# Optimization experiments

Measured on AMD Instinct MI355X. Metric: run time of the kernel, lower is better.

Reference implementation:

```python
import jax, jax.numpy as jnp
import numpy as np
from jax import lax

TOP_K = 4
N_GROUP = 4
TOPK_GROUP = 2
ROUTED_SCALE = 2.5
NEG_INF = -1e9


def setup_inputs() -> dict:
    key = jax.random.key(0)
    ks = jax.random.split(key, 6)
    B, S, H, I, E = 2, 2048, 1024, 512, 16
    x = jax.random.normal(ks[0], (B, S, H), dtype=jnp.float32)
    router_weight = jax.random.normal(ks[1], (E, H), dtype=jnp.float32) * 0.02
    router_bias = jnp.zeros((E,), dtype=jnp.float32)
    w_gate = jax.random.normal(ks[2], (E, I, H), dtype=jnp.float32) * 0.02
    w_up = jax.random.normal(ks[3], (E, I, H), dtype=jnp.float32) * 0.02
    w_down = jax.random.normal(ks[4], (E, H, I), dtype=jnp.float32) * 0.02
    return {"x": x, "router_weight": router_weight, "router_bias": router_bias,
            "w_gate": w_gate, "w_up": w_up, "w_down": w_down}


def _route(xf, router_weight, router_bias):
    # DeepSeek-V3 sigmoid router with group-limited top-k.
    T = xf.shape[0]
    E = router_weight.shape[0]
    logits = xf @ router_weight.T                      # [T, E]
    scores = jax.nn.sigmoid(logits)                    # [T, E]
    s_choice = scores + router_bias                    # bias used only for selection
    per_group = E // N_GROUP
    sg = s_choice.reshape(T, N_GROUP, per_group)
    group_scores = lax.top_k(sg, 2)[0].sum(-1)         # [T, n_group] sum of top-2
    _, gidx = lax.top_k(group_scores, TOPK_GROUP)      # [T, topk_group]
    gmask = jnp.zeros((T, N_GROUP), dtype=bool).at[jnp.arange(T)[:, None], gidx].set(True)
    masked = jnp.where(gmask[:, :, None], sg, NEG_INF).reshape(T, E)
    _, topk_idx = lax.top_k(masked, TOP_K)             # [T, top_k]
    w = jnp.take_along_axis(scores, topk_idx, axis=1)  # original sigmoid scores
    w = w / (w.sum(-1, keepdims=True) + 1e-20) * ROUTED_SCALE
    combine = jnp.zeros((T, E), dtype=xf.dtype).at[jnp.arange(T)[:, None], topk_idx].add(w)
    return combine


def reference(x, router_weight, router_bias, w_gate, w_up, w_down):
    B, S, H = x.shape
    E = w_gate.shape[0]
    xf = x.reshape(-1, H)                              # [T, H]
    combine = _route(xf, router_weight, router_bias)   # [T, E]
    # Grouped-GEMM SwiGLU experts expressed as per-expert dense GEMMs with
    # combine-weighted accumulation (same math as sort+grouped-mm+scatter).
    out = jnp.zeros_like(xf)
    for e in range(E):
        g = xf @ w_gate[e].T                           # [T, I]
        u = xf @ w_up[e].T                             # [T, I]
        y_e = (jax.nn.silu(g) * u) @ w_down[e].T       # [T, H]
        out = out + combine[:, e:e + 1] * y_e
    return out.reshape(B, S, H)
```

## Files before the change

kernel.cpp:

```cpp
#include <hip/hip_runtime.h>
#include <stdint.h>

#define T_TOK   4096
#define H_DIM   1024
#define I_DIM   512
#define E_EXP   16
#define TOPK    4
#define NTILEMAX 144

typedef __attribute__((ext_vector_type(8))) short bf16x8;
typedef __attribute__((ext_vector_type(4))) float f32x4;
typedef __attribute__((ext_vector_type(8))) unsigned short ushort8;

__device__ __forceinline__ unsigned short f2bf(float f) {
  unsigned u = __float_as_uint(f);
  u = u + 0x7fffu + ((u >> 16) & 1u);
  return (unsigned short)(u >> 16);
}
__device__ __forceinline__ float bf2f(unsigned short s) {
  return __uint_as_float(((unsigned)s) << 16);
}

__device__ __forceinline__ unsigned cvtpk(float lo, float hi) {
  unsigned r;
  asm("v_cvt_pk_bf16_f32 %0, %1, %2" : "=v"(r) : "v"(lo), "v"(hi));
  return r;
}

__device__ __forceinline__ void gload_lds16(const void* g, void* l) {
  __builtin_amdgcn_global_load_lds(
      (const __attribute__((address_space(1))) unsigned int*)g,
      (__attribute__((address_space(3))) unsigned int*)l, 16, 0, 0);
}

__global__ __launch_bounds__(256) void cvt_wd_kernel(
    const float* __restrict__ wd, unsigned short* __restrict__ wdb) {
  const int tid0 = blockIdx.x * blockDim.x + threadIdx.x;
  const int stride = gridDim.x * blockDim.x;
  const int n8 = E_EXP * H_DIM * I_DIM / 8;
  for (int i = tid0; i < n8; i += stride) {
    float4 v0 = ((const float4*)wd)[2 * i];
    float4 v1 = ((const float4*)wd)[2 * i + 1];
    ushort8 o;
    o[0] = f2bf(v0.x); o[1] = f2bf(v0.y); o[2] = f2bf(v0.z); o[3] = f2bf(v0.w);
    o[4] = f2bf(v1.x); o[5] = f2bf(v1.y); o[6] = f2bf(v1.z); o[7] = f2bf(v1.w);
    ((ushort8*)wdb)[i] = o;
  }
}

__global__ __launch_bounds__(256) void logits_sel_kernel(
    const float* __restrict__ x, const float* __restrict__ rw,
    const float* __restrict__ rb, unsigned short* __restrict__ xb,
    int* __restrict__ tidx, float* __restrict__ tw) {
  const int t = blockIdx.x * 4 + (threadIdx.x >> 6);
  const int lane = threadIdx.x & 63;
  const float* xr = x + (size_t)t * H_DIM;

  float4 xv[4];
#pragma unroll
  for (int i = 0; i < 4; ++i) xv[i] = ((const float4*)xr)[i * 64 + lane];

  unsigned short* xrow = xb + (size_t)t * H_DIM;
#pragma unroll
  for (int i = 0; i < 4; ++i) {
    ushort4 o;
    o.x = f2bf(xv[i].x); o.y = f2bf(xv[i].y);
    o.z = f2bf(xv[i].z); o.w = f2bf(xv[i].w);
    ((ushort4*)xrow)[i * 64 + lane] = o;
  }

  float myl[E_EXP];
#pragma unroll
  for (int g = 0; g < 4; ++g) {
    float acc[4] = {0.f, 0.f, 0.f, 0.f};
#pragma unroll
    for (int e4 = 0; e4 < 4; ++e4) {
      const float* wrow = rw + (size_t)(g * 4 + e4) * H_DIM;
#pragma unroll
      for (int i = 0; i < 4; ++i) {
        float4 wv = ((const float4*)wrow)[i * 64 + lane];
        acc[e4] = fmaf(xv[i].x, wv.x, acc[e4]);
        acc[e4] = fmaf(xv[i].y, wv.y, acc[e4]);
        acc[e4] = fmaf(xv[i].z, wv.z, acc[e4]);
        acc[e4] = fmaf(xv[i].w, wv.w, acc[e4]);
      }
    }
#pragma unroll
    for (int e4 = 0; e4 < 4; ++e4) {
#pragma unroll
      for (int off = 32; off > 0; off >>= 1) acc[e4] += __shfl_down(acc[e4], off, 64);
      myl[g * 4 + e4] = acc[e4];
    }
  }
  if (lane != 0) return;

  float sc[E_EXP], sch[E_EXP];
#pragma unroll
  for (int e = 0; e < E_EXP; ++e) {
    sc[e] = 1.f / (1.f + expf(-myl[e]));
    sch[e] = sc[e] + rb[e];
  }

  float gsum[4];
#pragma unroll
  for (int g = 0; g < 4; ++g) {
    float m1 = -3e38f, m2 = -3e38f;
#pragma unroll
    for (int j = 0; j < 4; ++j) {
      float v = sch[g * 4 + j];
      if (v > m1) { m2 = m1; m1 = v; } else if (v > m2) { m2 = v; }
    }
    gsum[g] = m1 + m2;
  }
  int g1 = 0;
  for (int g = 1; g < 4; ++g) if (gsum[g] > gsum[g1]) g1 = g;
  int g2 = -1;
  for (int g = 0; g < 4; ++g)
    if (g != g1 && (g2 < 0 || gsum[g] > gsum[g2])) g2 = g;

  float cand[E_EXP];
#pragma unroll
  for (int e = 0; e < E_EXP; ++e)
    cand[e] = ((e >> 2) == g1 || (e >> 2) == g2) ? sch[e] : -1e9f;

  int idx[TOPK]; float wv[TOPK]; float wsum = 0.f;
#pragma unroll
  for (int k = 0; k < TOPK; ++k) {
    int bi = 0; float bv = cand[0];
#pragma unroll
    for (int e = 1; e < E_EXP; ++e) if (cand[e] > bv) { bv = cand[e]; bi = e; }
    idx[k] = bi; cand[bi] = -3e38f;
    wv[k] = sc[bi];
    wsum += wv[k];
  }
  float scale = 2.5f / (wsum + 1e-20f);
#pragma unroll
  for (int k = 0; k < TOPK; ++k) {
    tidx[t * 4 + k] = idx[k];
    tw[t * 4 + k] = wv[k] * scale;
  }
}

__global__ __launch_bounds__(256) void plan_kernel(
    const int* __restrict__ tidx, int* __restrict__ offg,
    int* __restrict__ toffg, int* __restrict__ rowmap,
    int* __restrict__ rowtok) {
  const int e = blockIdx.x, tid = threadIdx.x;
  const int lane = tid & 63, wv = tid >> 6;
  __shared__ int histo[E_EXP];
  __shared__ int wsum[4];
  __shared__ int srun;
  if (tid < E_EXP) histo[tid] = 0;
  if (tid == 0) srun = 0;
  __syncthreads();
  for (int i = tid; i < T_TOK * TOPK; i += 256)
    atomicAdd(&histo[tidx[i]], 1);
  __syncthreads();

  if (e == 0 && tid == 0) {
    int a = 0, tt = 0;
    for (int q = 0; q < E_EXP; ++q) {
      offg[q] = a; toffg[q] = tt;
      a += histo[q];
      tt += (histo[q] + 127) >> 7;
    }
    offg[E_EXP] = a; toffg[E_EXP] = tt;
  }
  int base = 0;
  for (int q = 0; q < e; ++q) base += histo[q];

  for (int c = 0; c < T_TOK * TOPK / 256; ++c) {
    const int i = c * 256 + tid;
    const bool f = (tidx[i] == e);
    unsigned long long m = __ballot(f);
    int wpre = __popcll(m & ((1ull << lane) - 1ull));
    if (lane == 63) wsum[wv] = wpre + (f ? 1 : 0);
    __syncthreads();
    const int run = srun;
    int pre = 0, tot = 0;
#pragma unroll
    for (int w = 0; w < 4; ++w) {
      int v = wsum[w];
      if (w < wv) pre += v;
      tot += v;
    }
    if (f) {
      const int pos = base + run + pre + wpre;
      rowmap[i] = pos;
      rowtok[pos] = i >> 2;
    }
    __syncthreads();
    if (tid == 0) srun = run + tot;
  }
}

__device__ __forceinline__ int find_expert(const int* __restrict__ toff, int tile) {
  int e = 0;
#pragma unroll
  for (int q = 1; q <= E_EXP; ++q) e += (toff[q] <= tile);
  return e;
}

__global__ __launch_bounds__(256, 3) void gateup_kernel(
    const unsigned short* __restrict__ xbf,
    const float* __restrict__ wgf,
    const float* __restrict__ wuf,
    const int* __restrict__ rowtok, const int* __restrict__ off,
    const int* __restrict__ toff,
    unsigned short* __restrict__ hbuf) {
  const int bid = (int)blockIdx.x;
  const int work = (bid & 7) * NTILEMAX + (bid >> 3);
  const int tile = work >> 3, tn = work & 7;
  if (tile >= toff[E_EXP]) return;
  const int e = find_expert(toff, tile);
  const int tm = tile - toff[e];
  const int seg0 = off[e];
  const int nrows = off[e + 1] - seg0;

  __shared__ __align__(16) unsigned short As[128 * 64];
  __shared__ __align__(16) unsigned short Gs[64 * 64];
  __shared__ __align__(16) unsigned short Us[64 * 64];
  __shared__ int ids[128];

  const int tid = threadIdx.x;
  if (tid < 128) {
    int r = tm * 128 + tid;
    ids[tid] = rowtok[seg0 + (r < nrows ? r : 0)];
  }
  __syncthreads();

  const int col8 = tid & 7;
  const int r0 = tid >> 3;
  const int csrc = (col8 ^ (r0 & 7)) * 8;
  const int bcol = col8 * 8;
  const int bdst = (col8 ^ (r0 & 7)) * 8;
  int tokA[4];
#pragma unroll
  for (int j = 0; j < 4; ++j) tokA[j] = ids[j * 32 + r0];

  const float* wg = wgf + (size_t)e * I_DIM * H_DIM + (size_t)(tn * 64) * H_DIM;
  const float* wu = wuf + (size_t)e * I_DIM * H_DIM + (size_t)(tn * 64) * H_DIM;

  f32x4 accg[4][2], accu[4][2];
#pragma unroll
  for (int m = 0; m < 4; ++m)
#pragma unroll
    for (int n = 0; n < 2; ++n) { accg[m][n] = (f32x4)0.f; accu[m][n] = (f32x4)0.f; }

  const int lane = tid & 63, wid = tid >> 6;
  const int wr = wid >> 1, wc = wid & 1;
  const int frow = lane & 15, fr7 = frow & 7;
  const int kc = lane >> 4;

  const int NT = H_DIM / 64;
  float4 Bg[2][2], Bu[2][2];

  auto loadB = [&](int kt) {
#pragma unroll
    for (int j = 0; j < 2; ++j) {
      const float* gs = wg + (size_t)(j * 32 + r0) * H_DIM + kt * 64 + bcol;
      const float* us = wu + (size_t)(j * 32 + r0) * H_DIM + kt * 64 + bcol;
      Bg[j][0] = ((const float4*)gs)[0]; Bg[j][1] = ((const float4*)gs)[1];
      Bu[j][0] = ((const float4*)us)[0]; Bu[j][1] = ((const float4*)us)[1];
    }
  };

  loadB(0);
  for (int kt = 0; kt < NT; ++kt) {
    const int kbA = kt * 64 + csrc;
#pragma unroll
    for (int j = 0; j < 4; ++j)
      gload_lds16(xbf + ((size_t)tokA[j] * H_DIM + kbA), (char*)As + (j * 256 + tid) * 16);
#pragma unroll
    for (int j = 0; j < 2; ++j) {
      const int row = j * 32 + r0;
      uint4 gw, uw;
      gw.x = cvtpk(Bg[j][0].x, Bg[j][0].y); gw.y = cvtpk(Bg[j][0].z, Bg[j][0].w);
      gw.z = cvtpk(Bg[j][1].x, Bg[j][1].y); gw.w = cvtpk(Bg[j][1].z, Bg[j][1].w);
      uw.x = cvtpk(Bu[j][0].x, Bu[j][0].y); uw.y = cvtpk(Bu[j][0].z, Bu[j][0].w);
      uw.z = cvtpk(Bu[j][1].x, Bu[j][1].y); uw.w = cvtpk(Bu[j][1].z, Bu[j][1].w);
      *(uint4*)&Gs[row * 64 + bdst] = gw;
      *(uint4*)&Us[row * 64 + bdst] = uw;
    }
    __syncthreads();
    if (kt + 1 < NT) loadB(kt + 1);
    __builtin_amdgcn_sched_barrier(0);
#pragma unroll
    for (int kk = 0; kk < 2; ++kk) {
      const int swz = ((kk * 4 + kc) ^ fr7) * 8;
      bf16x8 af[4], bg[2], bu[2];
#pragma unroll
      for (int m = 0; m < 4; ++m)
        af[m] = *(const bf16x8*)&As[(wr * 64 + m * 16 + frow) * 64 + swz];
#pragma unroll
      for (int n = 0; n < 2; ++n) {
        bg[n] = *(const bf16x8*)&Gs[(wc * 32 + n * 16 + frow) * 64 + swz];
        bu[n] = *(const bf16x8*)&Us[(wc * 32 + n * 16 + frow) * 64 + swz];
      }
#pragma unroll
      for (int m = 0; m < 4; ++m)
#pragma unroll
        for (int n = 0; n < 2; ++n) {
          accg[m][n] = __builtin_amdgcn_mfma_f32_16x16x32_bf16(af[m], bg[n], accg[m][n], 0, 0, 0);
          accu[m][n] = __builtin_amdgcn_mfma_f32_16x16x32_bf16(af[m], bu[n], accu[m][n], 0, 0, 0);
        }
    }
    __builtin_amdgcn_sched_barrier(0);
    __builtin_amdgcn_s_barrier();
    __builtin_amdgcn_sched_barrier(0);
  }

  const int lr = (lane >> 4) * 4, lc = lane & 15;
#pragma unroll
  for (int m = 0; m < 4; ++m) {
#pragma unroll
    for (int j = 0; j < 4; ++j) {
      int r = tm * 128 + wr * 64 + m * 16 + lr + j;
      if (r < nrows) {
        size_t rowoff = (size_t)(seg0 + r) * I_DIM;
#pragma unroll
        for (int n = 0; n < 2; ++n) {
          float g = accg[m][n][j];
          float u = accu[m][n][j];
          float hv = g / (1.f + __expf(-g)) * u;
          hbuf[rowoff + tn * 64 + wc * 32 + n * 16 + lc] = f2bf(hv);
        }
      }
    }
  }
}

__global__ __launch_bounds__(256, 3) void down_kernel(
    const unsigned short* __restrict__ hbuf,
    const unsigned short* __restrict__ wdbf,
    const int* __restrict__ off, const int* __restrict__ toff,
    unsigned short* __restrict__ ybuf) {
  const int bid = (int)blockIdx.x;
  const int work = (bid & 7) * NTILEMAX + (bid >> 3);
  const int tile = work >> 3, tn = work & 7;
  if (tile >= toff[E_EXP]) return;
  const int e = find_expert(toff, tile);
  const int tm = tile - toff[e];
  const int seg0 = off[e];
  const int nrows = off[e + 1] - seg0;

  __shared__ __align__(16) unsigned short As[128 * 64];
  __shared__ __align__(16) unsigned short Bs[128 * 64];

  const int tid = threadIdx.x;
  const int col8 = tid & 7;
  const int r0 = tid >> 3;
  const int csrc = (col8 ^ (r0 & 7)) * 8;
  int rowA[4];
#pragma unroll
  for (int j = 0; j < 4; ++j) {
    int r = tm * 128 + j * 32 + r0;
    rowA[j] = seg0 + (r < nrows ? r : nrows - 1);
  }
  const unsigned short* wd = wdbf + (size_t)e * H_DIM * I_DIM + (size_t)(tn * 128) * I_DIM;

  f32x4 acc[4][4];
#pragma unroll
  for (int m = 0; m < 4; ++m)
#pragma unroll
    for (int n = 0; n < 4; ++n) acc[m][n] = (f32x4)0.f;

  const int lane = tid & 63, wid = tid >> 6;
  const int wr = wid >> 1, wc = wid & 1;
  const int frow = lane & 15, fr7 = frow & 7;
  const int kc = lane >> 4;

  for (int kt = 0; kt < I_DIM / 64; ++kt) {
    const int kb = kt * 64 + csrc;
    __syncthreads();
#pragma unroll
    for (int j = 0; j < 4; ++j) {
      gload_lds16(hbuf + ((size_t)rowA[j] * I_DIM + kb), (char*)As + (j * 256 + tid) * 16);
      gload_lds16(wd + ((size_t)(j * 32 + r0) * I_DIM + kb), (char*)Bs + (j * 256 + tid) * 16);
    }
    __syncthreads();
#pragma unroll
    for (int kk = 0; kk < 2; ++kk) {
      const int swz = ((kk * 4 + kc) ^ fr7) * 8;
      bf16x8 af[4], bw[4];
#pragma unroll
      for (int m = 0; m < 4; ++m)
        af[m] = *(const bf16x8*)&As[(wr * 64 + m * 16 + frow) * 64 + swz];
#pragma unroll
      for (int n = 0; n < 4; ++n)
        bw[n] = *(const bf16x8*)&Bs[(wc * 64 + n * 16 + frow) * 64 + swz];
#pragma unroll
      for (int m = 0; m < 4; ++m)
#pragma unroll
        for (int n = 0; n < 4; ++n)
          acc[m][n] = __builtin_amdgcn_mfma_f32_16x16x32_bf16(af[m], bw[n], acc[m][n], 0, 0, 0);
    }
  }

  const int lr = (lane >> 4) * 4, lc = lane & 15;
#pragma unroll
  for (int m = 0; m < 4; ++m) {
#pragma unroll
    for (int j = 0; j < 4; ++j) {
      int r = tm * 128 + wr * 64 + m * 16 + lr + j;
      if (r < nrows) {
        size_t rowoff = (size_t)(seg0 + r) * H_DIM;
#pragma unroll
        for (int n = 0; n < 4; ++n)
          ybuf[rowoff + tn * 128 + wc * 64 + n * 16 + lc] = f2bf(acc[m][n][j]);
      }
    }
  }
}

__global__ __launch_bounds__(256) void combine_kernel(
    const unsigned short* __restrict__ ybuf, const int* __restrict__ rowmap,
    const float* __restrict__ tw, float* __restrict__ out) {
  int t = blockIdx.x, tid = threadIdx.x;
  __shared__ int rloc[4];
  __shared__ float wloc[4];
  if (tid < 4) { rloc[tid] = rowmap[t * 4 + tid]; wloc[tid] = tw[t * 4 + tid]; }
  __syncthreads();
  int c = tid * 4;
  float4 a = {0.f, 0.f, 0.f, 0.f};
#pragma unroll
  for (int k = 0; k < 4; ++k) {
    ushort4 v = *(const ushort4*)&ybuf[(size_t)rloc[k] * H_DIM + c];
    float w = wloc[k];
    a.x += w * bf2f(v.x); a.y += w * bf2f(v.y);
    a.z += w * bf2f(v.z); a.w += w * bf2f(v.w);
  }
  *(float4*)&out[(size_t)t * H_DIM + c] = a;
}

extern "C" void kernel_launch(void* const* d_in, const int* in_sizes, int n_in,
                              void* d_out, int out_size, void* d_ws, size_t ws_size,
                              hipStream_t stream) {
  (void)in_sizes; (void)n_in; (void)out_size; (void)ws_size;
  const float* x  = (const float*)d_in[0];
  const float* rw = (const float*)d_in[1];
  const float* rb = (const float*)d_in[2];
  const float* wg = (const float*)d_in[3];
  const float* wu = (const float*)d_in[4];
  const float* wd = (const float*)d_in[5];
  float* out = (float*)d_out;

  char* base = (char*)d_ws;
  size_t o = 0;
  auto alloc = [&](size_t b) -> void* {
    void* p = base + o;
    o += (b + 255) & ~(size_t)255;
    return p;
  };
  unsigned short* xbf   = (unsigned short*)alloc((size_t)T_TOK * H_DIM * 2);
  unsigned short* wdbf  = (unsigned short*)alloc((size_t)E_EXP * H_DIM * I_DIM * 2);
  unsigned short* hbuf  = (unsigned short*)alloc((size_t)T_TOK * TOPK * I_DIM * 2);
  unsigned short* ybuf  = (unsigned short*)alloc((size_t)T_TOK * TOPK * H_DIM * 2);
  int*   tidx   = (int*)alloc((size_t)T_TOK * TOPK * 4);
  float* tw     = (float*)alloc((size_t)T_TOK * TOPK * 4);
  int*   rowmap = (int*)alloc((size_t)T_TOK * TOPK * 4);
  int*   rowtok = (int*)alloc((size_t)T_TOK * TOPK * 4);
  int*   offb   = (int*)alloc(256);
  int*   toffb  = (int*)alloc(256);

  cvt_wd_kernel<<<2048, 256, 0, stream>>>(wd, wdbf);
  logits_sel_kernel<<<T_TOK / 4, 256, 0, stream>>>(x, rw, rb, xbf, tidx, tw);
  plan_kernel<<<E_EXP, 256, 0, stream>>>(tidx, offb, toffb, rowmap, rowtok);

  gateup_kernel<<<8 * NTILEMAX, 256, 0, stream>>>(xbf, wg, wu, rowtok, offb, toffb, hbuf);
  down_kernel<<<8 * NTILEMAX, 256, 0, stream>>>(hbuf, wdbf, offb, toffb, ybuf);
  combine_kernel<<<T_TOK, 256, 0, stream>>>(ybuf, rowmap, tw, out);
}
```

Measured before the change: 159.2 us.

## Double M-tile to 256 rows and convert down weights in-kernel

Raises the per-block row tile from 128 to 256 in both expert GEMMs, so each block reuses every weight tile across twice as many tokens, and gives each wave a full 64-row strip with more accumulators. The separate fp32-to-bf16 conversion pass over the down-projection weights is removed. The down kernel now loads fp32 weights into registers one step ahead and converts them into shared memory, as the gate/up kernel already does. This costs more registers and LDS (occupancy hint drops to 2), leaves fewer blocks, and wastes more padding rows on small experts.

```diff
diff --git a/kernel.cpp b/kernel.cpp
--- a/kernel.cpp
+++ b/kernel.cpp
@@ -6,11 +6,10 @@
 #define I_DIM   512
 #define E_EXP   16
 #define TOPK    4
-#define NTILEMAX 144
+#define TILEMAX 80
 
 typedef __attribute__((ext_vector_type(8))) short bf16x8;
 typedef __attribute__((ext_vector_type(4))) float f32x4;
-typedef __attribute__((ext_vector_type(8))) unsigned short ushort8;
 
 __device__ __forceinline__ unsigned short f2bf(float f) {
   unsigned u = __float_as_uint(f);
@@ -31,21 +30,6 @@
   __builtin_amdgcn_global_load_lds(
       (const __attribute__((address_space(1))) unsigned int*)g,
       (__attribute__((address_space(3))) unsigned int*)l, 16, 0, 0);
-}
-
-__global__ __launch_bounds__(256) void cvt_wd_kernel(
-    const float* __restrict__ wd, unsigned short* __restrict__ wdb) {
-  const int tid0 = blockIdx.x * blockDim.x + threadIdx.x;
-  const int stride = gridDim.x * blockDim.x;
-  const int n8 = E_EXP * H_DIM * I_DIM / 8;
-  for (int i = tid0; i < n8; i += stride) {
-    float4 v0 = ((const float4*)wd)[2 * i];
-    float4 v1 = ((const float4*)wd)[2 * i + 1];
-    ushort8 o;
-    o[0] = f2bf(v0.x); o[1] = f2bf(v0.y); o[2] = f2bf(v0.z); o[3] = f2bf(v0.w);
-    o[4] = f2bf(v1.x); o[5] = f2bf(v1.y); o[6] = f2bf(v1.z); o[7] = f2bf(v1.w);
-    ((ushort8*)wdb)[i] = o;
-  }
 }
 
 __global__ __launch_bounds__(256) void logits_sel_kernel(
@@ -162,7 +146,7 @@
     for (int q = 0; q < E_EXP; ++q) {
       offg[q] = a; toffg[q] = tt;
       a += histo[q];
-      tt += (histo[q] + 127) >> 7;
+      tt += (histo[q] + 255) >> 8;
     }
     offg[E_EXP] = a; toffg[E_EXP] = tt;
   }
@@ -201,7 +185,7 @@
   return e;
 }
 
-__global__ __launch_bounds__(256, 3) void gateup_kernel(
+__global__ __launch_bounds__(256, 2) void gateup_kernel(
     const unsigned short* __restrict__ xbf,
     const float* __restrict__ wgf,
     const float* __restrict__ wuf,
@@ -209,7 +193,7 @@
     const int* __restrict__ toff,
     unsigned short* __restrict__ hbuf) {
   const int bid = (int)blockIdx.x;
-  const int work = (bid & 7) * NTILEMAX + (bid >> 3);
+  const int work = (bid & 7) * TILEMAX + (bid >> 3);
   const int tile = work >> 3, tn = work & 7;
   if (tile >= toff[E_EXP]) return;
   const int e = find_expert(toff, tile);
@@ -217,14 +201,14 @@
   const int seg0 = off[e];
   const int nrows = off[e + 1] - seg0;
 
-  __shared__ __align__(16) unsigned short As[128 * 64];
+  __shared__ __align__(16) unsigned short As[256 * 64];
   __shared__ __align__(16) unsigned short Gs[64 * 64];
   __shared__ __align__(16) unsigned short Us[64 * 64];
-  __shared__ int ids[128];
+  __shared__ int ids[256];
 
   const int tid = threadIdx.x;
-  if (tid < 128) {
-    int r = tm * 128 + tid;
+  {
+    int r = tm * 256 + tid;
     ids[tid] = rowtok[seg0 + (r < nrows ? r : 0)];
   }
   __syncthreads();
@@ -234,21 +218,20 @@
   const int csrc = (col8 ^ (r0 & 7)) * 8;
   const int bcol = col8 * 8;
   const int bdst = (col8 ^ (r0 & 7)) * 8;
-  int tokA[4];
-#pragma unroll
-  for (int j = 0; j < 4; ++j) tokA[j] = ids[j * 32 + r0];
+  int tokA[8];
+#pragma unroll
+  for (int j = 0; j < 8; ++j) tokA[j] = ids[j * 32 + r0];
 
   const float* wg = wgf + (size_t)e * I_DIM * H_DIM + (size_t)(tn * 64) * H_DIM;
   const float* wu = wuf + (size_t)e * I_DIM * H_DIM + (size_t)(tn * 64) * H_DIM;
 
-  f32x4 accg[4][2], accu[4][2];
+  f32x4 accg[4][4], accu[4][4];
 #pragma unroll
   for (int m = 0; m < 4; ++m)
 #pragma unroll
-    for (int n = 0; n < 2; ++n) { accg[m][n] = (f32x4)0.f; accu[m][n] = (f32x4)0.f; }
+    for (int n = 0; n < 4; ++n) { accg[m][n] = (f32x4)0.f; accu[m][n] = (f32x4)0.f; }
 
   const int lane = tid & 63, wid = tid >> 6;
-  const int wr = wid >> 1, wc = wid & 1;
   const int frow = lane & 15, fr7 = frow & 7;
   const int kc = lane >> 4;
 
@@ -269,7 +252,7 @@
   for (int kt = 0; kt < NT; ++kt) {
     const int kbA = kt * 64 + csrc;
 #pragma unroll
-    for (int j = 0; j < 4; ++j)
+    for (int j = 0; j < 8; ++j)
       gload_lds16(xbf + ((size_t)tokA[j] * H_DIM + kbA), (char*)As + (j * 256 + tid) * 16);
 #pragma unroll
     for (int j = 0; j < 2; ++j) {
@@ -288,19 +271,19 @@
 #pragma unroll
     for (int kk = 0; kk < 2; ++kk) {
       const int swz = ((kk * 4 + kc) ^ fr7) * 8;
-      bf16x8 af[4], bg[2], bu[2];
+      bf16x8 af[4], bg[4], bu[4];
 #pragma unroll
       for (int m = 0; m < 4; ++m)
-        af[m] = *(const bf16x8*)&As[(wr * 64 + m * 16 + frow) * 64 + swz];
-#pragma unroll
-      for (int n = 0; n < 2; ++n) {
-        bg[n] = *(const bf16x8*)&Gs[(wc * 32 + n * 16 + frow) * 64 + swz];
-        bu[n] = *(const bf16x8*)&Us[(wc * 32 + n * 16 + frow) * 64 + swz];
+        af[m] = *(const bf16x8*)&As[(wid * 64 + m * 16 + frow) * 64 + swz];
+#pragma unroll
+      for (int n = 0; n < 4; ++n) {
+        bg[n] = *(const bf16x8*)&Gs[(n * 16 + frow) * 64 + swz];
+        bu[n] = *(const bf16x8*)&Us[(n * 16 + frow) * 64 + swz];
       }
 #pragma unroll
       for (int m = 0; m < 4; ++m)
 #pragma unroll
-        for (int n = 0; n < 2; ++n) {
+        for (int n = 0; n < 4; ++n) {
           accg[m][n] = __builtin_amdgcn_mfma_f32_16x16x32_bf16(af[m], bg[n], accg[m][n], 0, 0, 0);
           accu[m][n] = __builtin_amdgcn_mfma_f32_16x16x32_bf16(af[m], bu[n], accu[m][n], 0, 0, 0);
         }
@@ -315,28 +298,28 @@
   for (int m = 0; m < 4; ++m) {
 #pragma unroll
     for (int j = 0; j < 4; ++j) {
-      int r = tm * 128 + wr * 64 + m * 16 + lr + j;
+      int r = tm * 256 + wid * 64 + m * 16 + lr + j;
       if (r < nrows) {
         size_t rowoff = (size_t)(seg0 + r) * I_DIM;
 #pragma unroll
-        for (int n = 0; n < 2; ++n) {
+        for (int n = 0; n < 4; ++n) {
           float g = accg[m][n][j];
           float u = accu[m][n][j];
           float hv = g / (1.f + __expf(-g)) * u;
-          hbuf[rowoff + tn * 64 + wc * 32 + n * 16 + lc] = f2bf(hv);
+          hbuf[rowoff + tn * 64 + n * 16 + lc] = f2bf(hv);
         }
       }
     }
   }
 }
 
-__global__ __launch_bounds__(256, 3) void down_kernel(
+__global__ __launch_bounds__(256, 2) void down_kernel(
     const unsigned short* __restrict__ hbuf,
-    const unsigned short* __restrict__ wdbf,
+    const float* __restrict__ wdf,
     const int* __restrict__ off, const int* __restrict__ toff,
     unsigned short* __restrict__ ybuf) {
   const int bid = (int)blockIdx.x;
-  const int work = (bid & 7) * NTILEMAX + (bid >> 3);
+  const int work = (bid & 7) * TILEMAX + (bid >> 3);
   const int tile = work >> 3, tn = work & 7;
   if (tile >= toff[E_EXP]) return;
   const int e = find_expert(toff, tile);
@@ -344,57 +327,85 @@
   const int seg0 = off[e];
   const int nrows = off[e + 1] - seg0;
 
-  __shared__ __align__(16) unsigned short As[128 * 64];
+  __shared__ __align__(16) unsigned short As[256 * 64];
   __shared__ __align__(16) unsigned short Bs[128 * 64];
+  __shared__ int ids[256];
 
   const int tid = threadIdx.x;
+  {
+    int r = tm * 256 + tid;
+    ids[tid] = seg0 + (r < nrows ? r : nrows - 1);
+  }
+  __syncthreads();
+
   const int col8 = tid & 7;
   const int r0 = tid >> 3;
   const int csrc = (col8 ^ (r0 & 7)) * 8;
-  int rowA[4];
-#pragma unroll
-  for (int j = 0; j < 4; ++j) {
-    int r = tm * 128 + j * 32 + r0;
-    rowA[j] = seg0 + (r < nrows ? r : nrows - 1);
-  }
-  const unsigned short* wd = wdbf + (size_t)e * H_DIM * I_DIM + (size_t)(tn * 128) * I_DIM;
-
-  f32x4 acc[4][4];
+  const int bcol = col8 * 8;
+  const int bdst = (col8 ^ (r0 & 7)) * 8;
+  int rowA[8];
+#pragma unroll
+  for (int j = 0; j < 8; ++j) rowA[j] = ids[j * 32 + r0];
+
+  const float* wd = wdf + (size_t)e * H_DIM * I_DIM + (size_t)(tn * 128) * I_DIM;
+
+  f32x4 acc[4][8];
 #pragma unroll
   for (int m = 0; m < 4; ++m)
 #pragma unroll
-    for (int n = 0; n < 4; ++n) acc[m][n] = (f32x4)0.f;
+    for (int n = 0; n < 8; ++n) acc[m][n] = (f32x4)0.f;
 
   const int lane = tid & 63, wid = tid >> 6;
-  const int wr = wid >> 1, wc = wid & 1;
   const int frow = lane & 15, fr7 = frow & 7;
   const int kc = lane >> 4;
 
-  for (int kt = 0; kt < I_DIM / 64; ++kt) {
-    const int kb = kt * 64 + csrc;
+  const int NT = I_DIM / 64;
+  float4 Bd[4][2];
+
+  auto loadB = [&](int kt) {
+#pragma unroll
+    for (int j = 0; j < 4; ++j) {
+      const float* ds = wd + (size_t)(j * 32 + r0) * I_DIM + kt * 64 + bcol;
+      Bd[j][0] = ((const float4*)ds)[0]; Bd[j][1] = ((const float4*)ds)[1];
+    }
+  };
+
+  loadB(0);
+  for (int kt = 0; kt < NT; ++kt) {
+    const int kbA = kt * 64 + csrc;
+#pragma unroll
+    for (int j = 0; j < 8; ++j)
+      gload_lds16(hbuf + ((size_t)rowA[j] * I_DIM + kbA), (char*)As + (j * 256 + tid) * 16);
+#pragma unroll
+    for (int j = 0; j < 4; ++j) {
+      const int row = j * 32 + r0;
+      uint4 w;
+      w.x = cvtpk(Bd[j][0].x, Bd[j][0].y); w.y = cvtpk(Bd[j][0].z, Bd[j][0].w);
+      w.z = cvtpk(Bd[j][1].x, Bd[j][1].y); w.w = cvtpk(Bd[j][1].z, Bd[j][1].w);
+      *(uint4*)&Bs[row * 64 + bdst] = w;
+    }
     __syncthreads();
-#pragma unroll
-    for (int j = 0; j < 4; ++j) {
-      gload_lds16(hbuf + ((size_t)rowA[j] * I_DIM + kb), (char*)As + (j * 256 + tid) * 16);
-      gload_lds16(wd + ((size_t)(j * 32 + r0) * I_DIM + kb), (char*)Bs + (j * 256 + tid) * 16);
-    }
-    __syncthreads();
+    if (kt + 1 < NT) loadB(kt + 1);
+    __builtin_amdgcn_sched_barrier(0);
 #pragma unroll
     for (int kk = 0; kk < 2; ++kk) {
       const int swz = ((kk * 4 + kc) ^ fr7) * 8;
-      bf16x8 af[4], bw[4];
+      bf16x8 af[4], bw[8];
 #pragma unroll
       for (int m = 0; m < 4; ++m)
-        af[m] = *(const bf16x8*)&As[(wr * 64 + m * 16 + frow) * 64 + swz];
-#pragma unroll
-      for (int n = 0; n < 4; ++n)
-        bw[n] = *(const bf16x8*)&Bs[(wc * 64 + n * 16 + frow) * 64 + swz];
+        af[m] = *(const bf16x8*)&As[(wid * 64 + m * 16 + frow) * 64 + swz];
+#pragma unroll
+      for (int n = 0; n < 8; ++n)
+        bw[n] = *(const bf16x8*)&Bs[(n * 16 + frow) * 64 + swz];
 #pragma unroll
       for (int m = 0; m < 4; ++m)
 #pragma unroll
-        for (int n = 0; n < 4; ++n)
+        for (int n = 0; n < 8; ++n)
           acc[m][n] = __builtin_amdgcn_mfma_f32_16x16x32_bf16(af[m], bw[n], acc[m][n], 0, 0, 0);
     }
+    __builtin_amdgcn_sched_barrier(0);
+    __builtin_amdgcn_s_barrier();
+    __builtin_amdgcn_sched_barrier(0);
   }
 
   const int lr = (lane >> 4) * 4, lc = lane & 15;
@@ -402,12 +413,12 @@
   for (int m = 0; m < 4; ++m) {
 #pragma unroll
     for (int j = 0; j < 4; ++j) {
-      int r = tm * 128 + wr * 64 + m * 16 + lr + j;
+      int r = tm * 256 + wid * 64 + m * 16 + lr + j;
       if (r < nrows) {
         size_t rowoff = (size_t)(seg0 + r) * H_DIM;
 #pragma unroll
-        for (int n = 0; n < 4; ++n)
-          ybuf[rowoff + tn * 128 + wc * 64 + n * 16 + lc] = f2bf(acc[m][n][j]);
+        for (int n = 0; n < 8; ++n)
+          ybuf[rowoff + tn * 128 + n * 16 + lc] = f2bf(acc[m][n][j]);
       }
     }
   }
@@ -453,7 +464,6 @@
     return p;
   };
   unsigned short* xbf   = (unsigned short*)alloc((size_t)T_TOK * H_DIM * 2);
-  unsigned short* wdbf  = (unsigned short*)alloc((size_t)E_EXP * H_DIM * I_DIM * 2);
   unsigned short* hbuf  = (unsigned short*)alloc((size_t)T_TOK * TOPK * I_DIM * 2);
   unsigned short* ybuf  = (unsigned short*)alloc((size_t)T_TOK * TOPK * H_DIM * 2);
   int*   tidx   = (int*)alloc((size_t)T_TOK * TOPK * 4);
@@ -463,11 +473,10 @@
   int*   offb   = (int*)alloc(256);
   int*   toffb  = (int*)alloc(256);
 
-  cvt_wd_kernel<<<2048, 256, 0, stream>>>(wd, wdbf);
   logits_sel_kernel<<<T_TOK / 4, 256, 0, stream>>>(x, rw, rb, xbf, tidx, tw);
   plan_kernel<<<E_EXP, 256, 0, stream>>>(tidx, offb, toffb, rowmap, rowtok);
 
-  gateup_kernel<<<8 * NTILEMAX, 256, 0, stream>>>(xbf, wg, wu, rowtok, offb, toffb, hbuf);
-  down_kernel<<<8 * NTILEMAX, 256, 0, stream>>>(hbuf, wdbf, offb, toffb, ybuf);
+  gateup_kernel<<<8 * TILEMAX, 256, 0, stream>>>(xbf, wg, wu, rowtok, offb, toffb, hbuf);
+  down_kernel<<<8 * TILEMAX, 256, 0, stream>>>(hbuf, wd, offb, toffb, ybuf);
   combine_kernel<<<T_TOK, 256, 0, stream>>>(ybuf, rowmap, tw, out);
 }
```

Measured after the change: 166.5 us, median of 2. 1.05x slower.
